# Kernel optimization log

Measured on AMD Instinct MI355X. Metric: run time of the kernel, lower is better.

## Reference

```python
import jax, jax.numpy as jnp
import numpy as np

NUM_CLASSES = 2
OVERLAP_THRESHOLD = 0.35
NEG_POS_RATIO = 7
VARIANCES = (0.1, 0.2)
B, P, G = 16, 131072, 32


def point_form(pri):
    # center form (cx,cy,w,h) -> corner form (x1,y1,x2,y2)
    return jnp.concatenate([pri[:, :2] - pri[:, 2:] / 2,
                            pri[:, :2] + pri[:, 2:] / 2], axis=1)


def jaccard(box_a, box_b):
    # box_a [G,4], box_b [P,4], corner form -> IoU [G,P]
    max_xy = jnp.minimum(box_a[:, None, 2:], box_b[None, :, 2:])
    min_xy = jnp.maximum(box_a[:, None, :2], box_b[None, :, :2])
    inter = jnp.prod(jnp.clip(max_xy - min_xy, 0.0, None), axis=2)
    area_a = jnp.prod(box_a[:, 2:] - box_a[:, :2], axis=1)[:, None]
    area_b = jnp.prod(box_b[:, 2:] - box_b[:, :2], axis=1)[None, :]
    return inter / (area_a + area_b - inter)


def encode(matched, pri, variances):
    g_cxcy = ((matched[:, :2] + matched[:, 2:]) / 2 - pri[:, :2]) / (variances[0] * pri[:, 2:])
    g_wh = jnp.log((matched[:, 2:] - matched[:, :2]) / pri[:, 2:]) / variances[1]
    return jnp.concatenate([g_cxcy, g_wh], axis=1)


def encode_landm(matched, pri, variances):
    m = matched.reshape(-1, 5, 2)  # [P,5,2]
    g = (m - pri[:, None, :2]) / (variances[0] * pri[:, None, 2:])
    return g.reshape(-1, 10)


def match_one(truths, landms, labels, pri):
    overlaps = jaccard(truths, point_form(pri))          # [G,P]
    best_prior_idx = jnp.argmax(overlaps, axis=1)        # [G] best prior per gt
    best_truth_overlap = jnp.max(overlaps, axis=0)       # [P]
    best_truth_idx = jnp.argmax(overlaps, axis=0)        # [P]
    # ensure each gt keeps its best prior
    best_truth_overlap = best_truth_overlap.at[best_prior_idx].set(2.0)
    best_truth_idx = best_truth_idx.at[best_prior_idx].set(jnp.arange(truths.shape[0]))
    matches = truths[best_truth_idx]                     # [P,4]
    conf = jnp.where(best_truth_overlap < OVERLAP_THRESHOLD, 0, labels[best_truth_idx])
    loc = encode(matches, pri, VARIANCES)
    landm = encode_landm(landms[best_truth_idx], pri, VARIANCES)
    return loc, conf, landm


def smooth_l1(pred, gt):
    d = jnp.abs(pred - gt)
    return jnp.where(d < 1.0, 0.5 * d * d, d - 0.5)


def multibox_loss(conf_data, loc_data, landm_data, priors, targets):
    batch_size, num_priors = loc_data.shape[0], priors.shape[0]
    truths = targets[:, :, :4]
    landms = targets[:, :, 4:14]
    labels = targets[:, :, 14].astype(jnp.int32)
    loc_t, conf_t, landm_t = jax.vmap(lambda t, l, lb: match_one(t, l, lb, priors))(truths, landms, labels)

    pos = conf_t > 0                                      # [B,P]
    num_pos_total = jnp.maximum(pos.sum().astype(loc_data.dtype), 1.0)
    num_pos_per_image = pos.sum(axis=1, keepdims=True)    # [B,1]
    posf = pos.astype(loc_data.dtype)

    loss_box = (smooth_l1(loc_data, loc_t).sum(-1) * posf).sum()
    loss_landm = (smooth_l1(landm_data, landm_t).sum(-1) * posf).sum()

    logp = jax.nn.log_softmax(conf_data, axis=-1)         # [B,P,C]
    ce = -jnp.take_along_axis(logp, jnp.clip(conf_t, 0, None)[..., None], axis=-1)[..., 0]
    loss_c = jnp.where(pos | (conf_t < 0), 0.0, ce)       # zero pos & ignored
    # hard negative mining: rank by descending loss via double argsort
    loss_idx = jnp.argsort(-loss_c, axis=1)
    idx_rank = jnp.argsort(loss_idx, axis=1)
    num_neg = jnp.minimum(NEG_POS_RATIO * num_pos_per_image, num_priors - 1)
    neg = idx_rank < num_neg
    pn = (pos | neg).astype(conf_data.dtype)
    loss_c_final = (ce * pn).sum()
    return (loss_box / num_pos_total, loss_c_final / num_pos_total, loss_landm / num_pos_total)


def setup_inputs() -> dict:
    key = jax.random.key(0)
    k1, k2, k3, k4, k5, k6, k7 = jax.random.split(key, 7)
    conf_data = jax.random.normal(k1, (B, P, NUM_CLASSES), dtype=jnp.float32)
    loc_data = jax.random.normal(k2, (B, P, 4), dtype=jnp.float32)
    landm_data = jax.random.normal(k3, (B, P, 10), dtype=jnp.float32)
    # priors in center form
    pc = jax.random.uniform(k4, (P, 2), minval=0.0, maxval=1.0)
    pwh = jax.random.uniform(k5, (P, 2), minval=0.02, maxval=0.3)
    priors = jnp.concatenate([pc, pwh], axis=1).astype(jnp.float32)
    # targets: [B,G,15] = corner box(4) + landms(10) + label(1)
    c = jax.random.uniform(k6, (B, G, 2), minval=0.2, maxval=0.8)
    s = jax.random.uniform(k7, (B, G, 2), minval=0.05, maxval=0.3)
    box = jnp.concatenate([c - s / 2, c + s / 2], axis=-1)
    lm = jax.random.uniform(jax.random.fold_in(key, 99), (B, G, 10), minval=0.0, maxval=1.0)
    lbl = jnp.ones((B, G, 1), dtype=jnp.float32)
    targets = jnp.concatenate([box, lm, lbl], axis=-1).astype(jnp.float32)
    return {"conf_data": conf_data, "loc_data": loc_data, "landm_data": landm_data,
            "priors": priors, "targets": targets}


def reference(conf_data, loc_data, landm_data, priors, targets):
    return multibox_loss(conf_data, loc_data, landm_data, priors, targets)
```

## Files before the change

kernel.cpp:

```cpp
#include <hip/hip_runtime.h>
#include <math.h>

#define B_ 16
#define P_ 131072
#define G_ 32
constexpr float OVER_THR = 0.35f;
constexpr float VAR0 = 0.1f;
constexpr float VAR1 = 0.2f;
constexpr int NEG_POS = 7;
constexpr int UNR = 8;
constexpr int LOSS_X = P_ / 256;
constexpr int LOSS_BLOCKS = LOSS_X * B_;
constexpr int NBIN13 = 8192;
constexpr int NBIN8 = 256;
constexpr int NBIN11 = 2048;
constexpr int SCAN_BLKS = 16;

__device__ inline float s1(float d) {
    d = fabsf(d);
    return d < 1.f ? 0.5f * d * d : d - 0.5f;
}

__device__ inline unsigned long long shfl_xor_u64(unsigned long long x, int m) {
    unsigned lo = (unsigned)x, hi = (unsigned)(x >> 32);
    lo = __shfl_xor(lo, m);
    hi = __shfl_xor(hi, m);
    return ((unsigned long long)hi << 32) | lo;
}

template <int NB>
__device__ void topk_select(const unsigned* __restrict__ h, unsigned rem,
                            int* out_bin, unsigned* out_rem) {
    constexpr int CHUNK = NB / 256;
    const int tid = threadIdx.x;
    unsigned cnt[CHUNK];
    unsigned csum = 0;
#pragma unroll
    for (int j = 0; j < CHUNK; ++j) { cnt[j] = h[tid * CHUNK + j]; csum += cnt[j]; }
    __shared__ unsigned ss[256];
    ss[tid] = csum;
    __syncthreads();
    for (int off = 1; off < 256; off <<= 1) {
        unsigned other = (tid + off < 256) ? ss[tid + off] : 0u;
        __syncthreads();
        ss[tid] += other;
        __syncthreads();
    }
    unsigned incl = ss[tid];
    unsigned excl = incl - csum;
    if (excl < rem && incl >= rem) {
        unsigned r = rem - excl, cum = 0;
        int selbin = tid * CHUNK;
#pragma unroll
        for (int j = CHUNK - 1; j >= 0; --j) {
            unsigned c = cnt[j];
            if (cum + c >= r) { selbin = tid * CHUNK + j; r = r - cum; break; }
            cum += c;
        }
        *out_bin = selbin;
        *out_rem = r;
    }
}

__global__ __launch_bounds__(256, 3) void k_match(
        const float4* __restrict__ priors4, const float* __restrict__ targets,
        unsigned char* __restrict__ bt, unsigned long long* __restrict__ pack) {
    const int b = blockIdx.y;
    const int base = blockIdx.x * (256 * UNR);
    const int tid = threadIdx.x;
    __shared__ unsigned long long red[G_][4];

    float px1[UNR], py1[UNR], px2[UNR], py2[UNR], pap[UNR], best[UNR];
    int bidx[UNR];
#pragma unroll
    for (int j = 0; j < UNR; ++j) {
        float4 pr = priors4[base + j * 256 + tid];
        px1[j] = pr.x - pr.z * 0.5f;  py1[j] = pr.y - pr.w * 0.5f;
        px2[j] = pr.x + pr.z * 0.5f;  py2[j] = pr.y + pr.w * 0.5f;
        pap[j] = pr.z * pr.w;
        best[j] = -1.0f; bidx[j] = 0;
    }
    const int lane = tid & 63, wave = tid >> 6;
    const float* tgb = targets + (size_t)b * G_ * 15;
#pragma unroll 1
    for (int g = 0; g < G_; ++g) {
        const float* tp = tgb + g * 15;
        float t0 = tp[0], t1 = tp[1], t2 = tp[2], t3 = tp[3];
        float ta = (t2 - t0) * (t3 - t1);
        float gb = -1.0f; int gj = 0;
#pragma unroll
        for (int j = 0; j < UNR; ++j) {
            float iw = fminf(t2, px2[j]) - fmaxf(t0, px1[j]);
            float ih = fminf(t3, py2[j]) - fmaxf(t1, py1[j]);
            float inter = fmaxf(iw, 0.f) * fmaxf(ih, 0.f);
            float iou = inter * __builtin_amdgcn_rcpf(ta + pap[j] - inter);
            if (iou > best[j]) { best[j] = iou; bidx[j] = g; }
            if (iou > gb) { gb = iou; gj = j; }
        }
        unsigned p = (unsigned)(base + (gj << 8) + tid);
        unsigned long long pk =
            ((unsigned long long)__float_as_uint(gb) << 32) | (unsigned)(~p);
#pragma unroll
        for (int off = 32; off > 0; off >>= 1) {
            unsigned long long o = shfl_xor_u64(pk, off);
            if (o > pk) pk = o;
        }
        if (lane == 0) red[g][wave] = pk;
    }
    __syncthreads();
    if (tid < G_) {
        unsigned long long m = red[tid][0];
#pragma unroll
        for (int w = 1; w < 4; ++w) if (red[tid][w] > m) m = red[tid][w];
        atomicMax(&pack[b * G_ + tid], m);
    }
#pragma unroll
    for (int j = 0; j < UNR; ++j) {
        int p = base + j * 256 + tid;
        bt[(size_t)b * P_ + p] =
            (unsigned char)(bidx[j] | (best[j] >= OVER_THR ? 64 : 0));
    }
}

__global__ void k_override(const unsigned long long* __restrict__ pack,
                           unsigned char* __restrict__ bt) {
    int b = threadIdx.x;
    if (b >= B_) return;
    for (int g = 0; g < G_; ++g) {
        unsigned long long pk = pack[b * G_ + g];
        unsigned p = ~(unsigned)(pk & 0xFFFFFFFFull);
        if (p < P_) bt[(size_t)b * P_ + p] = (unsigned char)(g | 64);
    }
}

__global__ __launch_bounds__(256) void k_loss(
        const float2* __restrict__ conf2, const float4* __restrict__ loc4,
        const float* __restrict__ landm, const float4* __restrict__ priors4,
        const float* __restrict__ targets,
        const unsigned char* __restrict__ bt,
        float* __restrict__ ce_neg,
        double* __restrict__ pb, double* __restrict__ pl,
        double* __restrict__ pc, int* __restrict__ pn) {
    const int b = blockIdx.y;
    const int p = blockIdx.x * 256 + threadIdx.x;
    const int tid = threadIdx.x;
    __shared__ float tg[G_ * 15];
    for (int i = tid; i < G_ * 15; i += 256) tg[i] = targets[(size_t)b * G_ * 15 + i];
    __syncthreads();

    const size_t gp = (size_t)b * P_ + p;
    unsigned char bv = bt[gp];
    int ti = bv & 63;
    bool thr_ok = (bv & 64) != 0;
    const float* t = &tg[ti * 15];
    float label = t[14];
    int conf_t = thr_ok ? (int)label : 0;
    bool pos = conf_t > 0;
    int cls = conf_t > 0 ? conf_t : 0;

    float2 c2 = conf2[gp];
    float mx = fmaxf(c2.x, c2.y);
    float lse = mx + logf(expf(c2.x - mx) + expf(c2.y - mx));
    float ce = lse - (cls ? c2.y : c2.x);
    ce_neg[gp] = (!pos && conf_t >= 0) ? ce : 0.f;

    float lb = 0.f, ll = 0.f;
    if (pos) {
        float4 pr = priors4[p];
        float vx = VAR0 * pr.z, vy = VAR0 * pr.w;
        float g0 = ((t[0] + t[2]) * 0.5f - pr.x) / vx;
        float g1 = ((t[1] + t[3]) * 0.5f - pr.y) / vy;
        float g2 = logf((t[2] - t[0]) / pr.z) / VAR1;
        float g3 = logf((t[3] - t[1]) / pr.w) / VAR1;
        float4 ld = loc4[gp];
        lb = s1(ld.x - g0) + s1(ld.y - g1) + s1(ld.z - g2) + s1(ld.w - g3);
        const float* lmp = landm + gp * 10;
#pragma unroll
        for (int i = 0; i < 5; ++i) {
            float2 lm = *(const float2*)(lmp + 2 * i);
            ll += s1(lm.x - (t[4 + 2 * i] - pr.x) / vx)
                + s1(lm.y - (t[5 + 2 * i] - pr.y) / vy);
        }
    }
    double vb = lb, vl = ll, vc = pos ? (double)ce : 0.0;
    int vp = pos ? 1 : 0;
#pragma unroll
    for (int off = 32; off > 0; off >>= 1) {
        vb += __shfl_xor(vb, off);
        vl += __shfl_xor(vl, off);
        vc += __shfl_xor(vc, off);
        vp += __shfl_xor(vp, off);
    }
    __shared__ double rb[4], rl[4], rc[4];
    __shared__ int rp[4];
    int lane = tid & 63, wave = tid >> 6;
    if (lane == 0) { rb[wave] = vb; rl[wave] = vl; rc[wave] = vc; rp[wave] = vp; }
    __syncthreads();
    if (tid == 0) {
        double sb = 0, sl = 0, sc = 0; int sp = 0;
        for (int w = 0; w < 4; ++w) { sb += rb[w]; sl += rl[w]; sc += rc[w]; sp += rp[w]; }
        int bi = blockIdx.y * LOSS_X + blockIdx.x;
        pb[bi] = sb; pl[bi] = sl; pc[bi] = sc; pn[bi] = sp;
    }
}

__global__ __launch_bounds__(1024) void k_hist13(
        const float* __restrict__ ce_neg, unsigned* __restrict__ hist) {
    const int b = blockIdx.y;
    const int tid = threadIdx.x;
    __shared__ unsigned h[NBIN13];
    for (int i = tid; i < NBIN13; i += 1024) h[i] = 0;
    __syncthreads();
    const float4* v4 = (const float4*)(ce_neg + (size_t)b * P_);
    const int c4 = P_ / SCAN_BLKS / 4;
    const int s4 = blockIdx.x * c4;
    for (int i = s4 + tid; i < s4 + c4; i += 1024) {
        float4 x = v4[i];
        atomicAdd(&h[__float_as_uint(x.x) >> 19], 1u);
        atomicAdd(&h[__float_as_uint(x.y) >> 19], 1u);
        atomicAdd(&h[__float_as_uint(x.z) >> 19], 1u);
        atomicAdd(&h[__float_as_uint(x.w) >> 19], 1u);
    }
    __syncthreads();
    unsigned* gh = hist + b * NBIN13;
    for (int i = tid; i < NBIN13; i += 1024)
        if (h[i]) atomicAdd(&gh[i], h[i]);
}

__global__ __launch_bounds__(256) void k_sel13(
        const unsigned* __restrict__ hist, const int* __restrict__ pn,
        int* __restrict__ sel, int* __restrict__ remk, int* __restrict__ npos) {
    const int b = blockIdx.x;
    const int tid = threadIdx.x;
    __shared__ int s_np;
    __shared__ int rnp[4];
    int loc = 0;
    for (int i = tid; i < LOSS_X; i += 256) loc += pn[b * LOSS_X + i];
#pragma unroll
    for (int off = 32; off > 0; off >>= 1) loc += __shfl_xor(loc, off);
    int lane = tid & 63, wave = tid >> 6;
    if (lane == 0) rnp[wave] = loc;
    __syncthreads();
    if (tid == 0) { int s = rnp[0] + rnp[1] + rnp[2] + rnp[3]; s_np = s; npos[b] = s; }
    __syncthreads();
    long long k = (long long)NEG_POS * s_np;
    if (k > P_ - 1) k = P_ - 1;
    if (k <= 0) { if (tid == 0) sel[b] = -1; return; }

    __shared__ int s_bin;
    __shared__ unsigned s_rem;
    topk_select<NBIN13>(hist + b * NBIN13, (unsigned)k, &s_bin, &s_rem);
    __syncthreads();
    if (tid == 0) { sel[b] = s_bin; remk[b] = (int)s_rem; }
}

__global__ __launch_bounds__(1024) void k_hist8(
        const float* __restrict__ ce_neg, const int* __restrict__ sel,
        unsigned* __restrict__ hist8) {
    const int b = blockIdx.y;
    const int s13 = sel[b];
    if (s13 < 0) return;
    const int tid = threadIdx.x;
    __shared__ unsigned h[NBIN8];
    if (tid < NBIN8) h[tid] = 0;
    __syncthreads();
    const float4* v4 = (const float4*)(ce_neg + (size_t)b * P_);
    const int c4 = P_ / SCAN_BLKS / 4;
    const int s4 = blockIdx.x * c4;
    for (int i = s4 + tid; i < s4 + c4; i += 1024) {
        float4 x = v4[i];
        unsigned u0 = __float_as_uint(x.x), u1 = __float_as_uint(x.y);
        unsigned u2 = __float_as_uint(x.z), u3 = __float_as_uint(x.w);
        if ((int)(u0 >> 19) == s13) atomicAdd(&h[(u0 >> 11) & 255u], 1u);
        if ((int)(u1 >> 19) == s13) atomicAdd(&h[(u1 >> 11) & 255u], 1u);
        if ((int)(u2 >> 19) == s13) atomicAdd(&h[(u2 >> 11) & 255u], 1u);
        if ((int)(u3 >> 19) == s13) atomicAdd(&h[(u3 >> 11) & 255u], 1u);
    }
    __syncthreads();
    if (tid < NBIN8 && h[tid]) atomicAdd(&hist8[b * NBIN8 + tid], h[tid]);
}

__global__ __launch_bounds__(256) void k_sel8(
        const unsigned* __restrict__ hist8, const int* __restrict__ sel,
        unsigned* __restrict__ pref, int* __restrict__ remk) {
    const int b = blockIdx.x;
    if (sel[b] < 0) return;
    __shared__ int s_bin;
    __shared__ unsigned s_rem;
    topk_select<NBIN8>(hist8 + b * NBIN8, (unsigned)remk[b], &s_bin, &s_rem);
    __syncthreads();
    if (threadIdx.x == 0) {
        pref[b] = ((unsigned)sel[b] << 8) | (unsigned)s_bin;
        remk[b] = (int)s_rem;
    }
}

__global__ __launch_bounds__(1024) void k_hist11(
        const float* __restrict__ ce_neg, const int* __restrict__ sel,
        const unsigned* __restrict__ pref, unsigned* __restrict__ hist11) {
    const int b = blockIdx.y;
    if (sel[b] < 0) return;
    const unsigned pf = pref[b];
    const int tid = threadIdx.x;
    __shared__ unsigned h[NBIN11];
    for (int i = tid; i < NBIN11; i += 1024) h[i] = 0;
    __syncthreads();
    const float4* v4 = (const float4*)(ce_neg + (size_t)b * P_);
    const int c4 = P_ / SCAN_BLKS / 4;
    const int s4 = blockIdx.x * c4;
    for (int i = s4 + tid; i < s4 + c4; i += 1024) {
        float4 x = v4[i];
        unsigned u0 = __float_as_uint(x.x), u1 = __float_as_uint(x.y);
        unsigned u2 = __float_as_uint(x.z), u3 = __float_as_uint(x.w);
        if ((u0 >> 11) == pf) atomicAdd(&h[u0 & 2047u], 1u);
        if ((u1 >> 11) == pf) atomicAdd(&h[u1 & 2047u], 1u);
        if ((u2 >> 11) == pf) atomicAdd(&h[u2 & 2047u], 1u);
        if ((u3 >> 11) == pf) atomicAdd(&h[u3 & 2047u], 1u);
    }
    __syncthreads();
    unsigned* gh = hist11 + b * NBIN11;
    for (int i = tid; i < NBIN11; i += 1024)
        if (h[i]) atomicAdd(&gh[i], h[i]);
}

__global__ __launch_bounds__(256) void k_sel11(
        const unsigned* __restrict__ hist11, const int* __restrict__ sel,
        const unsigned* __restrict__ pref, const int* __restrict__ remk,
        unsigned* __restrict__ thr, double* __restrict__ tot) {
    const int b = blockIdx.x;
    if (sel[b] < 0) { if (threadIdx.x == 0) thr[b] = 0xFFFFFFFFu; return; }
    __shared__ int s_bin;
    __shared__ unsigned s_rem;
    topk_select<NBIN11>(hist11 + b * NBIN11, (unsigned)remk[b], &s_bin, &s_rem);
    __syncthreads();
    if (threadIdx.x == 0) {
        unsigned t = (pref[b] << 11) | (unsigned)s_bin;
        thr[b] = t;
        atomicAdd(&tot[2], (double)s_rem * (double)__uint_as_float(t));
    }
}

__global__ __launch_bounds__(1024) void k_sumtop(
        const float* __restrict__ ce_neg, const unsigned* __restrict__ thr,
        double* __restrict__ tot) {
    const int b = blockIdx.y;
    const unsigned t = thr[b];
    if (t == 0xFFFFFFFFu) return;
    const int tid = threadIdx.x;
    const float4* v4 = (const float4*)(ce_neg + (size_t)b * P_);
    const int c4 = P_ / SCAN_BLKS / 4;
    const int s4 = blockIdx.x * c4;
    double loc = 0;
    for (int i = s4 + tid; i < s4 + c4; i += 1024) {
        float4 x = v4[i];
        if (__float_as_uint(x.x) > t) loc += x.x;
        if (__float_as_uint(x.y) > t) loc += x.y;
        if (__float_as_uint(x.z) > t) loc += x.z;
        if (__float_as_uint(x.w) > t) loc += x.w;
    }
#pragma unroll
    for (int off = 32; off > 0; off >>= 1) loc += __shfl_xor(loc, off);
    __shared__ double rs[16];
    int lane = tid & 63, wave = tid >> 6;
    if (lane == 0) rs[wave] = loc;
    __syncthreads();
    if (tid == 0) {
        double s = 0;
        for (int w = 0; w < 16; ++w) s += rs[w];
        atomicAdd(&tot[2], s);
    }
}

__global__ __launch_bounds__(1024) void k_final(
        const double* __restrict__ pb, const double* __restrict__ pl,
        const double* __restrict__ pc, const int* __restrict__ npos,
        const double* __restrict__ tot, float* __restrict__ out) {
    int tid = threadIdx.x;
    double sb = 0, sl = 0, sc = 0;
    for (int i = tid; i < LOSS_BLOCKS; i += 1024) {
        sb += pb[i]; sl += pl[i]; sc += pc[i];
    }
#pragma unroll
    for (int off = 32; off > 0; off >>= 1) {
        sb += __shfl_xor(sb, off);
        sl += __shfl_xor(sl, off);
        sc += __shfl_xor(sc, off);
    }
    __shared__ double rb[16], rl[16], rc[16];
    int lane = tid & 63, wave = tid >> 6;
    if (lane == 0) { rb[wave] = sb; rl[wave] = sl; rc[wave] = sc; }
    __syncthreads();
    if (tid == 0) {
        double b2 = 0, l2 = 0, c2 = 0;
        for (int w = 0; w < 16; ++w) { b2 += rb[w]; l2 += rl[w]; c2 += rc[w]; }
        long long tp = 0;
        for (int b = 0; b < B_; ++b) tp += npos[b];
        double n = tp > 0 ? (double)tp : 1.0;
        out[0] = (float)(b2 / n);
        out[1] = (float)((c2 + tot[2]) / n);
        out[2] = (float)(l2 / n);
    }
}

extern "C" void kernel_launch(void* const* d_in, const int* in_sizes, int n_in,
                              void* d_out, int out_size, void* d_ws, size_t ws_size,
                              hipStream_t stream) {
    const float* conf    = (const float*)d_in[0];
    const float* loc     = (const float*)d_in[1];
    const float* landm   = (const float*)d_in[2];
    const float* priors  = (const float*)d_in[3];
    const float* targets = (const float*)d_in[4];

    char* ws = (char*)d_ws;
    double* tot = (double*)ws;
    int* npos = (int*)(ws + 64);
    int* sel  = (int*)(ws + 128);
    int* remk = (int*)(ws + 192);
    unsigned* pref = (unsigned*)(ws + 256);
    unsigned* thr  = (unsigned*)(ws + 320);
    unsigned long long* pack = (unsigned long long*)(ws + 512);
    unsigned* hist13 = (unsigned*)(ws + 4608);
    unsigned* hist8  = hist13 + (size_t)B_ * NBIN13;
    unsigned* hist11 = hist8 + (size_t)B_ * NBIN8;
    size_t zero_bytes = 4608 + (size_t)B_ * (NBIN13 + NBIN8 + NBIN11) * 4;
    size_t big = (zero_bytes + 255) & ~(size_t)255;
    size_t BP = (size_t)B_ * P_;
    unsigned char* bt = (unsigned char*)(ws + big);
    float* ce_neg = (float*)(ws + big + BP);
    char* part = ws + big + BP * 5;
    double* pb = (double*)part;
    double* pl = (double*)(part + LOSS_BLOCKS * 8);
    double* pc = (double*)(part + LOSS_BLOCKS * 16);
    int*    pn = (int*)(part + LOSS_BLOCKS * 24);

    hipMemsetAsync(ws, 0, zero_bytes, stream);
    k_match<<<dim3(P_ / (256 * UNR), B_), 256, 0, stream>>>(
        (const float4*)priors, targets, bt, pack);
    k_override<<<1, 64, 0, stream>>>(pack, bt);
    k_loss<<<dim3(LOSS_X, B_), 256, 0, stream>>>(
        (const float2*)conf, (const float4*)loc, landm, (const float4*)priors,
        targets, bt, ce_neg, pb, pl, pc, pn);
    k_hist13<<<dim3(SCAN_BLKS, B_), 1024, 0, stream>>>(ce_neg, hist13);
    k_sel13<<<B_, 256, 0, stream>>>(hist13, pn, sel, remk, npos);
    k_hist8<<<dim3(SCAN_BLKS, B_), 1024, 0, stream>>>(ce_neg, sel, hist8);
    k_sel8<<<B_, 256, 0, stream>>>(hist8, sel, pref, remk);
    k_hist11<<<dim3(SCAN_BLKS, B_), 1024, 0, stream>>>(ce_neg, sel, pref, hist11);
    k_sel11<<<B_, 256, 0, stream>>>(hist11, sel, pref, remk, thr, tot);
    k_sumtop<<<dim3(SCAN_BLKS, B_), 1024, 0, stream>>>(ce_neg, thr, tot);
    k_final<<<1, 1024, 0, stream>>>(pb, pl, pc, npos, tot, (float*)d_out);
}
```

Before: 128.0 us.

## Fold per-batch select kernels into histogram kernels via last-block tickets

Removes the separate k_sel13, k_sel8, k_sel11 and k_final launches. Each histogram or sum kernel now uses a per-batch atomic ticket so that the last finishing block performs the threshold selection, or the final reduction, itself. This cuts four kernel launches and their serialization gaps. In exchange it adds threadfences and global atomics, and the selection scan now runs with 1024 threads in one of the scan blocks.

```diff
diff --git a/kernel.cpp b/kernel.cpp
--- a/kernel.cpp
+++ b/kernel.cpp
@@ -29,37 +29,40 @@
 }
 
 template <int NB>
-__device__ void topk_select(const unsigned* __restrict__ h, unsigned rem,
-                            int* out_bin, unsigned* out_rem) {
-    constexpr int CHUNK = NB / 256;
+__device__ void blk_select(const unsigned* __restrict__ gc, unsigned rem,
+                           int* sbin, unsigned* srem) {
+    constexpr int CHUNK = (NB + 1023) / 1024;
     const int tid = threadIdx.x;
     unsigned cnt[CHUNK];
     unsigned csum = 0;
 #pragma unroll
-    for (int j = 0; j < CHUNK; ++j) { cnt[j] = h[tid * CHUNK + j]; csum += cnt[j]; }
-    __shared__ unsigned ss[256];
+    for (int j = 0; j < CHUNK; ++j) {
+        int idx = tid * CHUNK + j;
+        unsigned c = (idx < NB) ? gc[idx] : 0u;
+        cnt[j] = c; csum += c;
+    }
+    __shared__ unsigned ss[1024];
     ss[tid] = csum;
     __syncthreads();
-    for (int off = 1; off < 256; off <<= 1) {
-        unsigned other = (tid + off < 256) ? ss[tid + off] : 0u;
-        __syncthreads();
-        ss[tid] += other;
-        __syncthreads();
-    }
-    unsigned incl = ss[tid];
-    unsigned excl = incl - csum;
+    for (int off = 1; off < 1024; off <<= 1) {
+        unsigned o = (tid + off < 1024) ? ss[tid + off] : 0u;
+        __syncthreads();
+        ss[tid] += o;
+        __syncthreads();
+    }
+    unsigned incl = ss[tid], excl = incl - csum;
     if (excl < rem && incl >= rem) {
         unsigned r = rem - excl, cum = 0;
-        int selbin = tid * CHUNK;
+        int sb_ = tid * CHUNK;
 #pragma unroll
         for (int j = CHUNK - 1; j >= 0; --j) {
             unsigned c = cnt[j];
-            if (cum + c >= r) { selbin = tid * CHUNK + j; r = r - cum; break; }
+            if (cum + c >= r) { sb_ = tid * CHUNK + j; r -= cum; break; }
             cum += c;
         }
-        *out_bin = selbin;
-        *out_rem = r;
-    }
+        *sbin = sb_; *srem = r;
+    }
+    __syncthreads();
 }
 
 __global__ __launch_bounds__(256, 3) void k_match(
@@ -205,7 +208,9 @@
 }
 
 __global__ __launch_bounds__(1024) void k_hist13(
-        const float* __restrict__ ce_neg, unsigned* __restrict__ hist) {
+        const float* __restrict__ ce_neg, unsigned* __restrict__ hist,
+        const int* __restrict__ pn, int* __restrict__ tick,
+        int* __restrict__ sel, int* __restrict__ remk, int* __restrict__ npos) {
     const int b = blockIdx.y;
     const int tid = threadIdx.x;
     __shared__ unsigned h[NBIN13];
@@ -225,157 +230,164 @@
     unsigned* gh = hist + b * NBIN13;
     for (int i = tid; i < NBIN13; i += 1024)
         if (h[i]) atomicAdd(&gh[i], h[i]);
-}
-
-__global__ __launch_bounds__(256) void k_sel13(
-        const unsigned* __restrict__ hist, const int* __restrict__ pn,
-        int* __restrict__ sel, int* __restrict__ remk, int* __restrict__ npos) {
-    const int b = blockIdx.x;
-    const int tid = threadIdx.x;
-    __shared__ int s_np;
-    __shared__ int rnp[4];
-    int loc = 0;
-    for (int i = tid; i < LOSS_X; i += 256) loc += pn[b * LOSS_X + i];
-#pragma unroll
-    for (int off = 32; off > 0; off >>= 1) loc += __shfl_xor(loc, off);
+    __threadfence();
+    __shared__ int amLast;
+    if (tid == 0) amLast = (atomicAdd(&tick[b], 1) == SCAN_BLKS - 1);
+    __syncthreads();
+    if (!amLast) return;
+    __threadfence();
+    int v = (tid < LOSS_X) ? pn[b * LOSS_X + tid] : 0;
+#pragma unroll
+    for (int off = 32; off > 0; off >>= 1) v += __shfl_xor(v, off);
+    __shared__ int rnp[16];
+    __shared__ long long s_k;
     int lane = tid & 63, wave = tid >> 6;
-    if (lane == 0) rnp[wave] = loc;
-    __syncthreads();
-    if (tid == 0) { int s = rnp[0] + rnp[1] + rnp[2] + rnp[3]; s_np = s; npos[b] = s; }
-    __syncthreads();
-    long long k = (long long)NEG_POS * s_np;
-    if (k > P_ - 1) k = P_ - 1;
+    if (lane == 0) rnp[wave] = v;
+    __syncthreads();
+    if (tid == 0) {
+        int s = 0;
+        for (int w = 0; w < 16; ++w) s += rnp[w];
+        npos[b] = s;
+        long long k = (long long)NEG_POS * s;
+        if (k > P_ - 1) k = P_ - 1;
+        s_k = k;
+    }
+    __syncthreads();
+    long long k = s_k;
     if (k <= 0) { if (tid == 0) sel[b] = -1; return; }
-
-    __shared__ int s_bin;
-    __shared__ unsigned s_rem;
-    topk_select<NBIN13>(hist + b * NBIN13, (unsigned)k, &s_bin, &s_rem);
-    __syncthreads();
-    if (tid == 0) { sel[b] = s_bin; remk[b] = (int)s_rem; }
+    __shared__ int sb_;
+    __shared__ unsigned sr_;
+    blk_select<NBIN13>(gh, (unsigned)k, &sb_, &sr_);
+    if (tid == 0) { sel[b] = sb_; remk[b] = (int)sr_; }
 }
 
 __global__ __launch_bounds__(1024) void k_hist8(
         const float* __restrict__ ce_neg, const int* __restrict__ sel,
-        unsigned* __restrict__ hist8) {
-    const int b = blockIdx.y;
+        unsigned* __restrict__ hist8, int* __restrict__ tick,
+        unsigned* __restrict__ pref, int* __restrict__ remk) {
+    const int b = blockIdx.y;
+    const int tid = threadIdx.x;
     const int s13 = sel[b];
-    if (s13 < 0) return;
-    const int tid = threadIdx.x;
-    __shared__ unsigned h[NBIN8];
-    if (tid < NBIN8) h[tid] = 0;
-    __syncthreads();
-    const float4* v4 = (const float4*)(ce_neg + (size_t)b * P_);
-    const int c4 = P_ / SCAN_BLKS / 4;
-    const int s4 = blockIdx.x * c4;
-    for (int i = s4 + tid; i < s4 + c4; i += 1024) {
-        float4 x = v4[i];
-        unsigned u0 = __float_as_uint(x.x), u1 = __float_as_uint(x.y);
-        unsigned u2 = __float_as_uint(x.z), u3 = __float_as_uint(x.w);
-        if ((int)(u0 >> 19) == s13) atomicAdd(&h[(u0 >> 11) & 255u], 1u);
-        if ((int)(u1 >> 19) == s13) atomicAdd(&h[(u1 >> 11) & 255u], 1u);
-        if ((int)(u2 >> 19) == s13) atomicAdd(&h[(u2 >> 11) & 255u], 1u);
-        if ((int)(u3 >> 19) == s13) atomicAdd(&h[(u3 >> 11) & 255u], 1u);
-    }
-    __syncthreads();
-    if (tid < NBIN8 && h[tid]) atomicAdd(&hist8[b * NBIN8 + tid], h[tid]);
-}
-
-__global__ __launch_bounds__(256) void k_sel8(
-        const unsigned* __restrict__ hist8, const int* __restrict__ sel,
-        unsigned* __restrict__ pref, int* __restrict__ remk) {
-    const int b = blockIdx.x;
-    if (sel[b] < 0) return;
-    __shared__ int s_bin;
-    __shared__ unsigned s_rem;
-    topk_select<NBIN8>(hist8 + b * NBIN8, (unsigned)remk[b], &s_bin, &s_rem);
-    __syncthreads();
-    if (threadIdx.x == 0) {
-        pref[b] = ((unsigned)sel[b] << 8) | (unsigned)s_bin;
-        remk[b] = (int)s_rem;
+    if (s13 >= 0) {
+        __shared__ unsigned h[NBIN8];
+        if (tid < NBIN8) h[tid] = 0;
+        __syncthreads();
+        const float4* v4 = (const float4*)(ce_neg + (size_t)b * P_);
+        const int c4 = P_ / SCAN_BLKS / 4;
+        const int s4 = blockIdx.x * c4;
+        for (int i = s4 + tid; i < s4 + c4; i += 1024) {
+            float4 x = v4[i];
+            unsigned u0 = __float_as_uint(x.x), u1 = __float_as_uint(x.y);
+            unsigned u2 = __float_as_uint(x.z), u3 = __float_as_uint(x.w);
+            if ((int)(u0 >> 19) == s13) atomicAdd(&h[(u0 >> 11) & 255u], 1u);
+            if ((int)(u1 >> 19) == s13) atomicAdd(&h[(u1 >> 11) & 255u], 1u);
+            if ((int)(u2 >> 19) == s13) atomicAdd(&h[(u2 >> 11) & 255u], 1u);
+            if ((int)(u3 >> 19) == s13) atomicAdd(&h[(u3 >> 11) & 255u], 1u);
+        }
+        __syncthreads();
+        if (tid < NBIN8 && h[tid]) atomicAdd(&hist8[b * NBIN8 + tid], h[tid]);
+    }
+    __threadfence();
+    __shared__ int amLast;
+    if (tid == 0) amLast = (atomicAdd(&tick[b], 1) == SCAN_BLKS - 1);
+    __syncthreads();
+    if (!amLast || s13 < 0) return;
+    __threadfence();
+    __shared__ int sb_;
+    __shared__ unsigned sr_;
+    blk_select<NBIN8>(hist8 + b * NBIN8, (unsigned)remk[b], &sb_, &sr_);
+    if (tid == 0) {
+        pref[b] = ((unsigned)s13 << 8) | (unsigned)sb_;
+        remk[b] = (int)sr_;
     }
 }
 
 __global__ __launch_bounds__(1024) void k_hist11(
         const float* __restrict__ ce_neg, const int* __restrict__ sel,
-        const unsigned* __restrict__ pref, unsigned* __restrict__ hist11) {
-    const int b = blockIdx.y;
-    if (sel[b] < 0) return;
-    const unsigned pf = pref[b];
-    const int tid = threadIdx.x;
-    __shared__ unsigned h[NBIN11];
-    for (int i = tid; i < NBIN11; i += 1024) h[i] = 0;
-    __syncthreads();
-    const float4* v4 = (const float4*)(ce_neg + (size_t)b * P_);
-    const int c4 = P_ / SCAN_BLKS / 4;
-    const int s4 = blockIdx.x * c4;
-    for (int i = s4 + tid; i < s4 + c4; i += 1024) {
-        float4 x = v4[i];
-        unsigned u0 = __float_as_uint(x.x), u1 = __float_as_uint(x.y);
-        unsigned u2 = __float_as_uint(x.z), u3 = __float_as_uint(x.w);
-        if ((u0 >> 11) == pf) atomicAdd(&h[u0 & 2047u], 1u);
-        if ((u1 >> 11) == pf) atomicAdd(&h[u1 & 2047u], 1u);
-        if ((u2 >> 11) == pf) atomicAdd(&h[u2 & 2047u], 1u);
-        if ((u3 >> 11) == pf) atomicAdd(&h[u3 & 2047u], 1u);
-    }
-    __syncthreads();
-    unsigned* gh = hist11 + b * NBIN11;
-    for (int i = tid; i < NBIN11; i += 1024)
-        if (h[i]) atomicAdd(&gh[i], h[i]);
-}
-
-__global__ __launch_bounds__(256) void k_sel11(
-        const unsigned* __restrict__ hist11, const int* __restrict__ sel,
-        const unsigned* __restrict__ pref, const int* __restrict__ remk,
+        const unsigned* __restrict__ pref, unsigned* __restrict__ hist11,
+        int* __restrict__ tick, const int* __restrict__ remk,
         unsigned* __restrict__ thr, double* __restrict__ tot) {
-    const int b = blockIdx.x;
-    if (sel[b] < 0) { if (threadIdx.x == 0) thr[b] = 0xFFFFFFFFu; return; }
-    __shared__ int s_bin;
-    __shared__ unsigned s_rem;
-    topk_select<NBIN11>(hist11 + b * NBIN11, (unsigned)remk[b], &s_bin, &s_rem);
-    __syncthreads();
-    if (threadIdx.x == 0) {
-        unsigned t = (pref[b] << 11) | (unsigned)s_bin;
+    const int b = blockIdx.y;
+    const int tid = threadIdx.x;
+    const int s13 = sel[b];
+    if (s13 >= 0) {
+        const unsigned pf = pref[b];
+        __shared__ unsigned h[NBIN11];
+        for (int i = tid; i < NBIN11; i += 1024) h[i] = 0;
+        __syncthreads();
+        const float4* v4 = (const float4*)(ce_neg + (size_t)b * P_);
+        const int c4 = P_ / SCAN_BLKS / 4;
+        const int s4 = blockIdx.x * c4;
+        for (int i = s4 + tid; i < s4 + c4; i += 1024) {
+            float4 x = v4[i];
+            unsigned u0 = __float_as_uint(x.x), u1 = __float_as_uint(x.y);
+            unsigned u2 = __float_as_uint(x.z), u3 = __float_as_uint(x.w);
+            if ((u0 >> 11) == pf) atomicAdd(&h[u0 & 2047u], 1u);
+            if ((u1 >> 11) == pf) atomicAdd(&h[u1 & 2047u], 1u);
+            if ((u2 >> 11) == pf) atomicAdd(&h[u2 & 2047u], 1u);
+            if ((u3 >> 11) == pf) atomicAdd(&h[u3 & 2047u], 1u);
+        }
+        __syncthreads();
+        unsigned* gh = hist11 + b * NBIN11;
+        for (int i = tid; i < NBIN11; i += 1024)
+            if (h[i]) atomicAdd(&gh[i], h[i]);
+    }
+    __threadfence();
+    __shared__ int amLast;
+    if (tid == 0) amLast = (atomicAdd(&tick[b], 1) == SCAN_BLKS - 1);
+    __syncthreads();
+    if (!amLast) return;
+    __threadfence();
+    if (s13 < 0) { if (tid == 0) thr[b] = 0xFFFFFFFFu; return; }
+    __shared__ int sb_;
+    __shared__ unsigned sr_;
+    blk_select<NBIN11>(hist11 + b * NBIN11, (unsigned)remk[b], &sb_, &sr_);
+    if (tid == 0) {
+        unsigned t = (pref[b] << 11) | (unsigned)sb_;
         thr[b] = t;
-        atomicAdd(&tot[2], (double)s_rem * (double)__uint_as_float(t));
+        atomicAdd(&tot[2], (double)sr_ * (double)__uint_as_float(t));
     }
 }
 
 __global__ __launch_bounds__(1024) void k_sumtop(
         const float* __restrict__ ce_neg, const unsigned* __restrict__ thr,
-        double* __restrict__ tot) {
-    const int b = blockIdx.y;
-    const unsigned t = thr[b];
-    if (t == 0xFFFFFFFFu) return;
-    const int tid = threadIdx.x;
-    const float4* v4 = (const float4*)(ce_neg + (size_t)b * P_);
-    const int c4 = P_ / SCAN_BLKS / 4;
-    const int s4 = blockIdx.x * c4;
-    double loc = 0;
-    for (int i = s4 + tid; i < s4 + c4; i += 1024) {
-        float4 x = v4[i];
-        if (__float_as_uint(x.x) > t) loc += x.x;
-        if (__float_as_uint(x.y) > t) loc += x.y;
-        if (__float_as_uint(x.z) > t) loc += x.z;
-        if (__float_as_uint(x.w) > t) loc += x.w;
-    }
-#pragma unroll
-    for (int off = 32; off > 0; off >>= 1) loc += __shfl_xor(loc, off);
-    __shared__ double rs[16];
-    int lane = tid & 63, wave = tid >> 6;
-    if (lane == 0) rs[wave] = loc;
-    __syncthreads();
-    if (tid == 0) {
-        double s = 0;
-        for (int w = 0; w < 16; ++w) s += rs[w];
-        atomicAdd(&tot[2], s);
-    }
-}
-
-__global__ __launch_bounds__(1024) void k_final(
+        double* __restrict__ tot, int* __restrict__ tickS,
         const double* __restrict__ pb, const double* __restrict__ pl,
         const double* __restrict__ pc, const int* __restrict__ npos,
-        const double* __restrict__ tot, float* __restrict__ out) {
-    int tid = threadIdx.x;
+        float* __restrict__ out) {
+    const int b = blockIdx.y;
+    const int tid = threadIdx.x;
+    const unsigned t = thr[b];
+    int lane = tid & 63, wave = tid >> 6;
+    if (t != 0xFFFFFFFFu) {
+        const float4* v4 = (const float4*)(ce_neg + (size_t)b * P_);
+        const int c4 = P_ / SCAN_BLKS / 4;
+        const int s4 = blockIdx.x * c4;
+        double loc = 0;
+        for (int i = s4 + tid; i < s4 + c4; i += 1024) {
+            float4 x = v4[i];
+            if (__float_as_uint(x.x) > t) loc += x.x;
+            if (__float_as_uint(x.y) > t) loc += x.y;
+            if (__float_as_uint(x.z) > t) loc += x.z;
+            if (__float_as_uint(x.w) > t) loc += x.w;
+        }
+#pragma unroll
+        for (int off = 32; off > 0; off >>= 1) loc += __shfl_xor(loc, off);
+        __shared__ double rs[16];
+        if (lane == 0) rs[wave] = loc;
+        __syncthreads();
+        if (tid == 0) {
+            double s = 0;
+            for (int w = 0; w < 16; ++w) s += rs[w];
+            atomicAdd(&tot[2], s);
+        }
+    }
+    __threadfence();
+    __shared__ int amLast;
+    if (tid == 0) amLast = (atomicAdd(tickS, 1) == SCAN_BLKS * B_ - 1);
+    __syncthreads();
+    if (!amLast) return;
+    __threadfence();
     double sb = 0, sl = 0, sc = 0;
     for (int i = tid; i < LOSS_BLOCKS; i += 1024) {
         sb += pb[i]; sl += pl[i]; sc += pc[i];
@@ -387,14 +399,13 @@
         sc += __shfl_xor(sc, off);
     }
     __shared__ double rb[16], rl[16], rc[16];
-    int lane = tid & 63, wave = tid >> 6;
     if (lane == 0) { rb[wave] = sb; rl[wave] = sl; rc[wave] = sc; }
     __syncthreads();
     if (tid == 0) {
         double b2 = 0, l2 = 0, c2 = 0;
         for (int w = 0; w < 16; ++w) { b2 += rb[w]; l2 += rl[w]; c2 += rc[w]; }
         long long tp = 0;
-        for (int b = 0; b < B_; ++b) tp += npos[b];
+        for (int i = 0; i < B_; ++i) tp += npos[i];
         double n = tp > 0 ? (double)tp : 1.0;
         out[0] = (float)(b2 / n);
         out[1] = (float)((c2 + tot[2]) / n);
@@ -418,11 +429,15 @@
     int* remk = (int*)(ws + 192);
     unsigned* pref = (unsigned*)(ws + 256);
     unsigned* thr  = (unsigned*)(ws + 320);
-    unsigned long long* pack = (unsigned long long*)(ws + 512);
-    unsigned* hist13 = (unsigned*)(ws + 4608);
+    int* tick1 = (int*)(ws + 384);
+    int* tick2 = (int*)(ws + 448);
+    int* tick3 = (int*)(ws + 512);
+    int* tickS = (int*)(ws + 576);
+    unsigned long long* pack = (unsigned long long*)(ws + 1024);
+    unsigned* hist13 = (unsigned*)(ws + 5120);
     unsigned* hist8  = hist13 + (size_t)B_ * NBIN13;
     unsigned* hist11 = hist8 + (size_t)B_ * NBIN8;
-    size_t zero_bytes = 4608 + (size_t)B_ * (NBIN13 + NBIN8 + NBIN11) * 4;
+    size_t zero_bytes = 5120 + (size_t)B_ * (NBIN13 + NBIN8 + NBIN11) * 4;
     size_t big = (zero_bytes + 255) & ~(size_t)255;
     size_t BP = (size_t)B_ * P_;
     unsigned char* bt = (unsigned char*)(ws + big);
@@ -440,12 +455,12 @@
     k_loss<<<dim3(LOSS_X, B_), 256, 0, stream>>>(
         (const float2*)conf, (const float4*)loc, landm, (const float4*)priors,
         targets, bt, ce_neg, pb, pl, pc, pn);
-    k_hist13<<<dim3(SCAN_BLKS, B_), 1024, 0, stream>>>(ce_neg, hist13);
-    k_sel13<<<B_, 256, 0, stream>>>(hist13, pn, sel, remk, npos);
-    k_hist8<<<dim3(SCAN_BLKS, B_), 1024, 0, stream>>>(ce_neg, sel, hist8);
-    k_sel8<<<B_, 256, 0, stream>>>(hist8, sel, pref, remk);
-    k_hist11<<<dim3(SCAN_BLKS, B_), 1024, 0, stream>>>(ce_neg, sel, pref, hist11);
-    k_sel11<<<B_, 256, 0, stream>>>(hist11, sel, pref, remk, thr, tot);
-    k_sumtop<<<dim3(SCAN_BLKS, B_), 1024, 0, stream>>>(ce_neg, thr, tot);
-    k_final<<<1, 1024, 0, stream>>>(pb, pl, pc, npos, tot, (float*)d_out);
-}
+    k_hist13<<<dim3(SCAN_BLKS, B_), 1024, 0, stream>>>(
+        ce_neg, hist13, pn, tick1, sel, remk, npos);
+    k_hist8<<<dim3(SCAN_BLKS, B_), 1024, 0, stream>>>(
+        ce_neg, sel, hist8, tick2, pref, remk);
+    k_hist11<<<dim3(SCAN_BLKS, B_), 1024, 0, stream>>>(
+        ce_neg, sel, pref, hist11, tick3, remk, thr, tot);
+    k_sumtop<<<dim3(SCAN_BLKS, B_), 1024, 0, stream>>>(
+        ce_neg, thr, tot, tickS, pb, pl, pc, npos, (float*)d_out);
+}
```

Result: slower. 382.4 us (+198.8%).

## Fold top-k sum into final histogram pass and drop separate sumtop scan

Applied to the files above, without the earlier changes.

The last radix-select histogram pass now also accumulates the sum of negatives whose 21-bit prefix lies above the selected prefix. The final select kernel adds the contributions of bins above the threshold bin, computed from the histogram counts times their exact float values, plus the tie remainder. This removes one full read of the ce_neg array and one kernel launch. In exchange it adds double accumulation and a block reduction to the histogram kernel.

```diff
diff --git a/kernel.cpp b/kernel.cpp
--- a/kernel.cpp
+++ b/kernel.cpp
@@ -297,7 +297,8 @@
 
 __global__ __launch_bounds__(1024) void k_hist11(
         const float* __restrict__ ce_neg, const int* __restrict__ sel,
-        const unsigned* __restrict__ pref, unsigned* __restrict__ hist11) {
+        const unsigned* __restrict__ pref, unsigned* __restrict__ hist11,
+        double* __restrict__ tot) {
     const int b = blockIdx.y;
     if (sel[b] < 0) return;
     const unsigned pf = pref[b];
@@ -308,65 +309,62 @@
     const float4* v4 = (const float4*)(ce_neg + (size_t)b * P_);
     const int c4 = P_ / SCAN_BLKS / 4;
     const int s4 = blockIdx.x * c4;
+    double above = 0;
     for (int i = s4 + tid; i < s4 + c4; i += 1024) {
         float4 x = v4[i];
         unsigned u0 = __float_as_uint(x.x), u1 = __float_as_uint(x.y);
         unsigned u2 = __float_as_uint(x.z), u3 = __float_as_uint(x.w);
-        if ((u0 >> 11) == pf) atomicAdd(&h[u0 & 2047u], 1u);
-        if ((u1 >> 11) == pf) atomicAdd(&h[u1 & 2047u], 1u);
-        if ((u2 >> 11) == pf) atomicAdd(&h[u2 & 2047u], 1u);
-        if ((u3 >> 11) == pf) atomicAdd(&h[u3 & 2047u], 1u);
+        unsigned h0 = u0 >> 11, h1 = u1 >> 11, h2 = u2 >> 11, h3 = u3 >> 11;
+        if (h0 == pf) atomicAdd(&h[u0 & 2047u], 1u); else if (h0 > pf) above += x.x;
+        if (h1 == pf) atomicAdd(&h[u1 & 2047u], 1u); else if (h1 > pf) above += x.y;
+        if (h2 == pf) atomicAdd(&h[u2 & 2047u], 1u); else if (h2 > pf) above += x.z;
+        if (h3 == pf) atomicAdd(&h[u3 & 2047u], 1u); else if (h3 > pf) above += x.w;
     }
     __syncthreads();
     unsigned* gh = hist11 + b * NBIN11;
     for (int i = tid; i < NBIN11; i += 1024)
         if (h[i]) atomicAdd(&gh[i], h[i]);
+#pragma unroll
+    for (int off = 32; off > 0; off >>= 1) above += __shfl_xor(above, off);
+    __shared__ double rs[16];
+    int lane = tid & 63, wave = tid >> 6;
+    if (lane == 0) rs[wave] = above;
+    __syncthreads();
+    if (tid == 0) {
+        double s = 0;
+        for (int w = 0; w < 16; ++w) s += rs[w];
+        atomicAdd(&tot[2], s);
+    }
 }
 
 __global__ __launch_bounds__(256) void k_sel11(
         const unsigned* __restrict__ hist11, const int* __restrict__ sel,
         const unsigned* __restrict__ pref, const int* __restrict__ remk,
-        unsigned* __restrict__ thr, double* __restrict__ tot) {
+        double* __restrict__ tot) {
     const int b = blockIdx.x;
-    if (sel[b] < 0) { if (threadIdx.x == 0) thr[b] = 0xFFFFFFFFu; return; }
+    if (sel[b] < 0) return;
+    const int tid = threadIdx.x;
     __shared__ int s_bin;
     __shared__ unsigned s_rem;
     topk_select<NBIN11>(hist11 + b * NBIN11, (unsigned)remk[b], &s_bin, &s_rem);
     __syncthreads();
-    if (threadIdx.x == 0) {
-        unsigned t = (pref[b] << 11) | (unsigned)s_bin;
-        thr[b] = t;
-        atomicAdd(&tot[2], (double)s_rem * (double)__uint_as_float(t));
-    }
-}
-
-__global__ __launch_bounds__(1024) void k_sumtop(
-        const float* __restrict__ ce_neg, const unsigned* __restrict__ thr,
-        double* __restrict__ tot) {
-    const int b = blockIdx.y;
-    const unsigned t = thr[b];
-    if (t == 0xFFFFFFFFu) return;
-    const int tid = threadIdx.x;
-    const float4* v4 = (const float4*)(ce_neg + (size_t)b * P_);
-    const int c4 = P_ / SCAN_BLKS / 4;
-    const int s4 = blockIdx.x * c4;
-    double loc = 0;
-    for (int i = s4 + tid; i < s4 + c4; i += 1024) {
-        float4 x = v4[i];
-        if (__float_as_uint(x.x) > t) loc += x.x;
-        if (__float_as_uint(x.y) > t) loc += x.y;
-        if (__float_as_uint(x.z) > t) loc += x.z;
-        if (__float_as_uint(x.w) > t) loc += x.w;
-    }
-#pragma unroll
-    for (int off = 32; off > 0; off >>= 1) loc += __shfl_xor(loc, off);
-    __shared__ double rs[16];
+    const unsigned pf = pref[b];
+    const unsigned* gh = hist11 + b * NBIN11;
+    double a = 0;
+    for (int i = s_bin + 1 + tid; i < NBIN11; i += 256) {
+        unsigned c = gh[i];
+        if (c) a += (double)c * (double)__uint_as_float((pf << 11) | (unsigned)i);
+    }
+#pragma unroll
+    for (int off = 32; off > 0; off >>= 1) a += __shfl_xor(a, off);
+    __shared__ double rs[4];
     int lane = tid & 63, wave = tid >> 6;
-    if (lane == 0) rs[wave] = loc;
+    if (lane == 0) rs[wave] = a;
     __syncthreads();
     if (tid == 0) {
-        double s = 0;
-        for (int w = 0; w < 16; ++w) s += rs[w];
+        unsigned T = (pf << 11) | (unsigned)s_bin;
+        double s = rs[0] + rs[1] + rs[2] + rs[3];
+        s += (double)s_rem * (double)__uint_as_float(T);
         atomicAdd(&tot[2], s);
     }
 }
@@ -417,7 +415,6 @@
     int* sel  = (int*)(ws + 128);
     int* remk = (int*)(ws + 192);
     unsigned* pref = (unsigned*)(ws + 256);
-    unsigned* thr  = (unsigned*)(ws + 320);
     unsigned long long* pack = (unsigned long long*)(ws + 512);
     unsigned* hist13 = (unsigned*)(ws + 4608);
     unsigned* hist8  = hist13 + (size_t)B_ * NBIN13;
@@ -444,8 +441,7 @@
     k_sel13<<<B_, 256, 0, stream>>>(hist13, pn, sel, remk, npos);
     k_hist8<<<dim3(SCAN_BLKS, B_), 1024, 0, stream>>>(ce_neg, sel, hist8);
     k_sel8<<<B_, 256, 0, stream>>>(hist8, sel, pref, remk);
-    k_hist11<<<dim3(SCAN_BLKS, B_), 1024, 0, stream>>>(ce_neg, sel, pref, hist11);
-    k_sel11<<<B_, 256, 0, stream>>>(hist11, sel, pref, remk, thr, tot);
-    k_sumtop<<<dim3(SCAN_BLKS, B_), 1024, 0, stream>>>(ce_neg, thr, tot);
+    k_hist11<<<dim3(SCAN_BLKS, B_), 1024, 0, stream>>>(ce_neg, sel, pref, hist11, tot);
+    k_sel11<<<B_, 256, 0, stream>>>(hist11, sel, pref, remk, tot);
     k_final<<<1, 1024, 0, stream>>>(pb, pl, pc, npos, tot, (float*)d_out);
 }
```

Result: no change. 126.8 us (-0.9%).
